# Kernel tuning notes

Measured on AMD Instinct MI355X. Metric: run time of the kernel, lower is better.

The kernel has to match this reference:

```python
import jax, jax.numpy as jnp
import numpy as np

X_DIM = 40
N_BATCH = 65536


def _circ_conv1d(x, W, b, pad):
    # x: [N, C_in, L], W: [C_out, C_in, K] (torch layout), circular padding
    if pad > 0:
        x = jnp.pad(x, ((0, 0), (0, 0), (pad, pad)), mode='wrap')
    y = jax.lax.conv_general_dilated(x, W, window_strides=(1,), padding='VALID',
                                     dimension_numbers=('NCH', 'OIH', 'NCH'))
    return y + b[None, :, None]


def setup_inputs() -> dict:
    key = jax.random.key(0)
    ks = jax.random.split(key, 9)
    u = jax.random.normal(ks[0], (N_BATCH, X_DIM), dtype=jnp.float32)
    coeff = jax.random.normal(ks[1], (18,), dtype=jnp.float32) * 0.1
    # Conv1d params, torch layout [out_ch, in_ch, kernel], kaiming-ish scale
    W1 = jax.random.normal(ks[2], (72, 1, 5), dtype=jnp.float32) * (1.0 / np.sqrt(1 * 5))
    b1 = jax.random.normal(ks[3], (72,), dtype=jnp.float32) * 0.05
    W2 = jax.random.normal(ks[4], (37, 48, 5), dtype=jnp.float32) * (1.0 / np.sqrt(48 * 5))
    b2 = jax.random.normal(ks[5], (37,), dtype=jnp.float32) * 0.05
    W3 = jax.random.normal(ks[6], (1, 37, 1), dtype=jnp.float32) * (1.0 / np.sqrt(37))
    b3 = jax.random.normal(ks[7], (1,), dtype=jnp.float32) * 0.05
    t = jnp.zeros((1,), dtype=jnp.float32)  # unused by the module, kept for signature fidelity
    return {"t": t, "u": u, "coeff": coeff, "W1": W1, "b1": b1,
            "W2": W2, "b2": b2, "W3": W3, "b3": b3}


def reference(t, u, coeff, W1, b1, W2, b2, W3, b3):
    # circular neighbor gathers: index_select with (i+k)%D == roll by -k
    u_m2 = jnp.roll(u, 2, axis=-1)
    u_m1 = jnp.roll(u, 1, axis=-1)
    u_p1 = jnp.roll(u, -1, axis=-1)
    u_p2 = jnp.roll(u, -2, axis=-1)
    feats = jnp.stack([
        jnp.ones_like(u),
        u_m2, u_m1, u, u_p1, u_p2,
        u_m2 ** 2, u_m1 ** 2, u ** 2, u_p1 ** 2, u_p2 ** 2,
        u_m2 * u_m1, u_m1 * u, u * u_p1, u_p1 * u_p2,
        u_m2 * u, u_m1 * u_p1, u * u_p2,
    ], axis=-1)  # [N, D, 18]
    out1 = feats @ coeff  # [N, D]

    x = u[:, None, :]  # [N, 1, D]
    h = jax.nn.relu(_circ_conv1d(x, W1, b1, 2))  # [N, 72, D]
    h = jnp.concatenate([h[:, :24], h[:, 24:48] * h[:, 48:]], axis=1)  # [N, 48, D]
    h = jax.nn.relu(_circ_conv1d(h, W2, b2, 2))  # [N, 37, D]
    out2 = _circ_conv1d(h, W3, b3, 0)[:, 0, :]  # [N, D]
    return out1 + out2
```

## Files before the change

### kernel.cpp

```cpp
#include <hip/hip_runtime.h>
#include <hip/hip_bf16.h>

typedef short s16x8 __attribute__((ext_vector_type(8)));
typedef short s16x4 __attribute__((ext_vector_type(4)));
typedef float f32x4 __attribute__((ext_vector_type(4)));

#define TB 8
#define NBG 4
#define HALO 46
#define GSTRIDE 2216
#define USTRIDE 50
#define NT 3
#define GT_SHORTS (TB * GSTRIDE)

__device__ __forceinline__ unsigned short f2bf(float f) {
    unsigned int u = __float_as_uint(f);
    u += 0x7fff + ((u >> 16) & 1);
    return (unsigned short)(u >> 16);
}

__device__ __forceinline__ unsigned int pk_bf16(float lo, float hi) {
    float2 f; f.x = lo; f.y = hi;
    __hip_bfloat162 h = __float22bfloat162_rn(f);
    union { __hip_bfloat162 b; unsigned int u; } c;
    c.b = h;
    return c.u;
}

__global__ __launch_bounds__(256, 2) void lorenz96_fused(
    const float* __restrict__ u,
    const float* __restrict__ coeff,
    const float* __restrict__ W1,
    const float* __restrict__ b1,
    const float* __restrict__ W2,
    const float* __restrict__ b2,
    const float* __restrict__ W3,
    const float* __restrict__ b3,
    float* __restrict__ out)
{
    __shared__ __align__(16) unsigned short gtile[GT_SHORTS];
    __shared__ __align__(16) float u_sbuf[2][TB * USTRIDE];
    __shared__ float out1_s[TB * 40];

    unsigned short* B_lds = gtile;

    const int t    = threadIdx.x;
    const int lane = t & 63;
    const int wave = t >> 6;
    const int quad = lane >> 4;
    const int l15  = lane & 15;

    const int b0_block = blockIdx.x * (TB * NBG);

    for (int g = t; g < NT * 8 * 64; g += 256) {
        int lg = g & 63;
        int ks = (g >> 6) & 7;
        int nt = g >> 9;
        int o  = nt * 16 + (lg & 15);
        int kb = ks * 32 + (lg >> 4) * 8;
        s16x8 pack = {0, 0, 0, 0, 0, 0, 0, 0};
        #pragma unroll
        for (int j = 0; j < 8; ++j) {
            int k = kb + j;
            if (k < 240 && o < 37) {
                int c = k % 48, tap = k / 48;
                pack[j] = (short)f2bf(W2[o * 240 + c * 5 + tap]);
            }
        }
        *(s16x8*)&B_lds[g * 8] = pack;
    }

    for (int idx = t; idx < TB * USTRIDE; idx += 256) {
        int b = idx / USTRIDE, k = idx - b * USTRIDE;
        int gi = k + 36; gi -= (gi >= 40) ? 40 : 0; gi -= (gi >= 40) ? 40 : 0;
        u_sbuf[0][idx] = u[(size_t)(b0_block + b) * 40 + gi];
    }

    s16x8 aW1[5];
    {
        int chs[5];
        chs[0] = l15; chs[1] = 16 + l15; chs[2] = 32 + l15;
        chs[3] = (l15 >= 8) ? 40 + l15 : -1;
        chs[4] = 56 + l15;
        #pragma unroll
        for (int mt = 0; mt < 5; ++mt) {
            s16x8 a = {0, 0, 0, 0, 0, 0, 0, 0};
            int ch = chs[mt];
            if (quad == 0 && ch >= 0) {
                #pragma unroll
                for (int j = 0; j < 5; ++j) a[j] = (short)f2bf(W1[ch * 5 + j]);
                a[5] = (short)f2bf(b1[ch]);
            }
            aW1[mt] = a;
        }
    }

    float w3v[NT][4], b2v[NT][4];
    #pragma unroll
    for (int nt = 0; nt < NT; ++nt)
        #pragma unroll
        for (int r = 0; r < 4; ++r) {
            int o = nt * 16 + quad * 4 + r;
            bool valid = (o < 37);
            w3v[nt][r] = valid ? W3[o] : 0.f;
            b2v[nt][r] = valid ? b2[o] : 0.f;
        }
    const float b3v = b3[0];
    float cf[18];
    #pragma unroll
    for (int i = 0; i < 18; ++i) cf[i] = coeff[i];

    __syncthreads();

    s16x8 aW2[NT][8];
    #pragma unroll
    for (int nt = 0; nt < NT; ++nt)
        #pragma unroll
        for (int ks = 0; ks < 8; ++ks)
            aW2[nt][ks] = *(const s16x8*)&B_lds[((nt * 8 + ks) * 64 + lane) * 8];

    for (int grp = 0; grp < NBG; ++grp) {
        const int b0 = b0_block + grp * TB;
        const float* u_s = u_sbuf[grp & 1];

        __syncthreads();

        {
            #pragma unroll
            for (int pass = 0; pass < 2; ++pass) {
                int i = pass ? 4 : quad;
                bool act = pass ? (quad == 0) : true;
                if (act) {
                    int m = (wave + 4 * i) * 16 + l15;
                    int p = m >> 3, b = m & 7;
                    const float* us = &u_s[b * USTRIDE + p];
                    float um2 = us[2], um1 = us[3], u0 = us[4], up1 = us[5], up2 = us[6];
                    float r = cf[0] + cf[1]*um2 + cf[2]*um1 + cf[3]*u0 + cf[4]*up1 + cf[5]*up2
                            + cf[6]*um2*um2 + cf[7]*um1*um1 + cf[8]*u0*u0 + cf[9]*up1*up1 + cf[10]*up2*up2
                            + cf[11]*um2*um1 + cf[12]*um1*u0 + cf[13]*u0*up1 + cf[14]*up1*up2
                            + cf[15]*um2*u0 + cf[16]*um1*up1 + cf[17]*u0*up2;
                    out1_s[m] = r;
                }
            }
        }

        #pragma unroll
        for (int i = 0; i < 6; ++i) {
            const int ct  = wave + 4 * i;
            const int col = ct * 16 + l15;
            const int b = col & 7, h = col >> 3;
            const int hc = (h < HALO) ? h : 0;
            s16x8 bU = {0, 0, 0, 0, 0, 0, 0, 0};
            if (quad == 0) {
                const float* us = &u_s[b * USTRIDE + hc];
                union { s16x8 v; unsigned int w[4]; } bu;
                bu.w[0] = pk_bf16(us[0], us[1]);
                bu.w[1] = pk_bf16(us[2], us[3]);
                bu.w[2] = pk_bf16(us[4], 1.0f);
                bu.w[3] = 0;
                bU = bu.v;
            }
            f32x4 a0 = {0.f,0.f,0.f,0.f}, a1 = a0, a2 = a0, a3 = a0, a4 = a0;
            a0 = __builtin_amdgcn_mfma_f32_16x16x32_bf16(aW1[0], bU, a0, 0, 0, 0);
            a1 = __builtin_amdgcn_mfma_f32_16x16x32_bf16(aW1[1], bU, a1, 0, 0, 0);
            a2 = __builtin_amdgcn_mfma_f32_16x16x32_bf16(aW1[2], bU, a2, 0, 0, 0);
            a3 = __builtin_amdgcn_mfma_f32_16x16x32_bf16(aW1[3], bU, a3, 0, 0, 0);
            a4 = __builtin_amdgcn_mfma_f32_16x16x32_bf16(aW1[4], bU, a4, 0, 0, 0);
            if (h < HALO) {
                float v0[4], v1[4], v2[4];
                #pragma unroll
                for (int r = 0; r < 4; ++r) {
                    v0[r] = fmaxf(a0[r], 0.f);
                    v1[r] = fmaxf(a1[r], 0.f);
                    if (quad >= 2) v1[r] *= fmaxf(a3[r], 0.f);
                    v2[r] = fmaxf(a2[r], 0.f) * fmaxf(a4[r], 0.f);
                }
                union { s16x4 v; unsigned int w[2]; } w0, w1, w2;
                w0.w[0] = pk_bf16(v0[0], v0[1]); w0.w[1] = pk_bf16(v0[2], v0[3]);
                w1.w[0] = pk_bf16(v1[0], v1[1]); w1.w[1] = pk_bf16(v1[2], v1[3]);
                w2.w[0] = pk_bf16(v2[0], v2[1]); w2.w[1] = pk_bf16(v2[2], v2[3]);
                unsigned short* gp = &gtile[b * GSTRIDE + h * 48 + quad * 4];
                *(s16x4*)(gp)      = w0.v;
                *(s16x4*)(gp + 16) = w1.v;
                *(s16x4*)(gp + 32) = w2.v;
            }
        }

        if (grp + 1 < NBG) {
            for (int idx = t; idx < TB * USTRIDE; idx += 256) {
                int b = idx / USTRIDE, k = idx - b * USTRIDE;
                int gi = k + 36; gi -= (gi >= 40) ? 40 : 0; gi -= (gi >= 40) ? 40 : 0;
                u_sbuf[(grp + 1) & 1][idx] = u[(size_t)(b0 + TB + b) * 40 + gi];
            }
        }

        __syncthreads();

        #pragma unroll
        for (int i = 0; i < 5; ++i) {
            const int mt = wave + 4 * i;
            const int m  = mt * 16 + l15;
            const int p  = m >> 3, b = m & 7;
            const unsigned short* gbase = &gtile[b * GSTRIDE + p * 48 + quad * 8];
            s16x8 bg[8];
            #pragma unroll
            for (int ks = 0; ks < 8; ++ks) bg[ks] = *(const s16x8*)(gbase + ks * 32);
            f32x4 c0 = {0.f,0.f,0.f,0.f}, c1 = c0, c2 = c0;
            #pragma unroll
            for (int ks = 0; ks < 8; ++ks) {
                c0 = __builtin_amdgcn_mfma_f32_16x16x32_bf16(aW2[0][ks], bg[ks], c0, 0, 0, 0);
                c1 = __builtin_amdgcn_mfma_f32_16x16x32_bf16(aW2[1][ks], bg[ks], c1, 0, 0, 0);
                c2 = __builtin_amdgcn_mfma_f32_16x16x32_bf16(aW2[2][ks], bg[ks], c2, 0, 0, 0);
            }
            float s = 0.f;
            #pragma unroll
            for (int r = 0; r < 4; ++r) {
                s += fmaxf(c0[r] + b2v[0][r], 0.f) * w3v[0][r];
                s += fmaxf(c1[r] + b2v[1][r], 0.f) * w3v[1][r];
                s += fmaxf(c2[r] + b2v[2][r], 0.f) * w3v[2][r];
            }
            s += __shfl_xor(s, 16, 64);
            s += __shfl_xor(s, 32, 64);
            if (lane < 16) {
                int mo = mt * 16 + lane;
                out[(size_t)(b0 + (mo & 7)) * 40 + (mo >> 3)] = s + b3v + out1_s[mo];
            }
        }
    }
}

extern "C" void kernel_launch(void* const* d_in, const int* in_sizes, int n_in,
                              void* d_out, int out_size, void* d_ws, size_t ws_size,
                              hipStream_t stream) {
    const float* u     = (const float*)d_in[1];
    const float* coeff = (const float*)d_in[2];
    const float* W1    = (const float*)d_in[3];
    const float* b1    = (const float*)d_in[4];
    const float* W2    = (const float*)d_in[5];
    const float* b2    = (const float*)d_in[6];
    const float* W3    = (const float*)d_in[7];
    const float* b3    = (const float*)d_in[8];
    float* out = (float*)d_out;

    const int n_batch = in_sizes[1] / 40;
    const int grid = n_batch / (TB * NBG);
    lorenz96_fused<<<grid, 256, 0, stream>>>(u, coeff, W1, b1, W2, b2, W3, b3, out);
}
```

Baseline: 211.1 us.

## Double-buffer conv intermediate tile and fold conv2 bias into MFMA

Double-buffers the LDS intermediate tile and the polynomial output, so the next group's conv1 stage is computed right after the current group's conv2 stage. This leaves one barrier per group instead of two. The conv2 bias is folded into the weight fragment at reduction index 240, with a bf16 1.0 injected into the B operand, which drops the per-element bias add. Each block now handles 8 batch groups instead of 4, amortizing weight setup over more work. The cost is double the LDS footprint, which may limit occupancy, and half as many blocks.

```diff
diff --git a/kernel.cpp b/kernel.cpp
--- a/kernel.cpp
+++ b/kernel.cpp
@@ -6,7 +6,7 @@
 typedef float f32x4 __attribute__((ext_vector_type(4)));
 
 #define TB 8
-#define NBG 4
+#define NBG 8
 #define HALO 46
 #define GSTRIDE 2216
 #define USTRIDE 50
@@ -38,11 +38,11 @@
     const float* __restrict__ b3,
     float* __restrict__ out)
 {
-    __shared__ __align__(16) unsigned short gtile[GT_SHORTS];
+    __shared__ __align__(16) unsigned short gtile[2][GT_SHORTS];
     __shared__ __align__(16) float u_sbuf[2][TB * USTRIDE];
-    __shared__ float out1_s[TB * 40];
-
-    unsigned short* B_lds = gtile;
+    __shared__ float out1_sb[2][TB * 40];
+
+    unsigned short* B_lds = &gtile[0][0];
 
     const int t    = threadIdx.x;
     const int lane = t & 63;
@@ -62,18 +62,16 @@
         #pragma unroll
         for (int j = 0; j < 8; ++j) {
             int k = kb + j;
-            if (k < 240 && o < 37) {
-                int c = k % 48, tap = k / 48;
-                pack[j] = (short)f2bf(W2[o * 240 + c * 5 + tap]);
+            if (o < 37) {
+                if (k < 240) {
+                    int c = k % 48, tap = k / 48;
+                    pack[j] = (short)f2bf(W2[o * 240 + c * 5 + tap]);
+                } else if (k == 240) {
+                    pack[j] = (short)f2bf(b2[o]);
+                }
             }
         }
         *(s16x8*)&B_lds[g * 8] = pack;
-    }
-
-    for (int idx = t; idx < TB * USTRIDE; idx += 256) {
-        int b = idx / USTRIDE, k = idx - b * USTRIDE;
-        int gi = k + 36; gi -= (gi >= 40) ? 40 : 0; gi -= (gi >= 40) ? 40 : 0;
-        u_sbuf[0][idx] = u[(size_t)(b0_block + b) * 40 + gi];
     }
 
     s16x8 aW1[5];
@@ -95,55 +93,51 @@
         }
     }
 
-    float w3v[NT][4], b2v[NT][4];
+    float w3v[NT][4];
     #pragma unroll
     for (int nt = 0; nt < NT; ++nt)
         #pragma unroll
         for (int r = 0; r < 4; ++r) {
             int o = nt * 16 + quad * 4 + r;
-            bool valid = (o < 37);
-            w3v[nt][r] = valid ? W3[o] : 0.f;
-            b2v[nt][r] = valid ? b2[o] : 0.f;
+            w3v[nt][r] = (o < 37) ? W3[o] : 0.f;
         }
     const float b3v = b3[0];
     float cf[18];
     #pragma unroll
     for (int i = 0; i < 18; ++i) cf[i] = coeff[i];
 
-    __syncthreads();
-
-    s16x8 aW2[NT][8];
-    #pragma unroll
-    for (int nt = 0; nt < NT; ++nt)
-        #pragma unroll
-        for (int ks = 0; ks < 8; ++ks)
-            aW2[nt][ks] = *(const s16x8*)&B_lds[((nt * 8 + ks) * 64 + lane) * 8];
-
-    for (int grp = 0; grp < NBG; ++grp) {
-        const int b0 = b0_block + grp * TB;
+    auto prestage_u = [&](int grp) {
+        for (int idx = t; idx < TB * USTRIDE; idx += 256) {
+            int b = idx / USTRIDE, k = idx - b * USTRIDE;
+            int gi = k + 36; gi -= (gi >= 40) ? 40 : 0; gi -= (gi >= 40) ? 40 : 0;
+            u_sbuf[grp & 1][idx] = u[(size_t)(b0_block + grp * TB + b) * 40 + gi];
+        }
+    };
+
+    auto poly = [&](int grp) {
         const float* u_s = u_sbuf[grp & 1];
-
-        __syncthreads();
-
-        {
-            #pragma unroll
-            for (int pass = 0; pass < 2; ++pass) {
-                int i = pass ? 4 : quad;
-                bool act = pass ? (quad == 0) : true;
-                if (act) {
-                    int m = (wave + 4 * i) * 16 + l15;
-                    int p = m >> 3, b = m & 7;
-                    const float* us = &u_s[b * USTRIDE + p];
-                    float um2 = us[2], um1 = us[3], u0 = us[4], up1 = us[5], up2 = us[6];
-                    float r = cf[0] + cf[1]*um2 + cf[2]*um1 + cf[3]*u0 + cf[4]*up1 + cf[5]*up2
-                            + cf[6]*um2*um2 + cf[7]*um1*um1 + cf[8]*u0*u0 + cf[9]*up1*up1 + cf[10]*up2*up2
-                            + cf[11]*um2*um1 + cf[12]*um1*u0 + cf[13]*u0*up1 + cf[14]*up1*up2
-                            + cf[15]*um2*u0 + cf[16]*um1*up1 + cf[17]*u0*up2;
-                    out1_s[m] = r;
-                }
-            }
-        }
-
+        float* o1 = out1_sb[grp & 1];
+        #pragma unroll
+        for (int pass = 0; pass < 2; ++pass) {
+            int i = pass ? 4 : quad;
+            bool act = pass ? (quad == 0) : true;
+            if (act) {
+                int m = (wave + 4 * i) * 16 + l15;
+                int p = m >> 3, b = m & 7;
+                const float* us = &u_s[b * USTRIDE + p];
+                float um2 = us[2], um1 = us[3], u0 = us[4], up1 = us[5], up2 = us[6];
+                float r = cf[0] + cf[1]*um2 + cf[2]*um1 + cf[3]*u0 + cf[4]*up1 + cf[5]*up2
+                        + cf[6]*um2*um2 + cf[7]*um1*um1 + cf[8]*u0*u0 + cf[9]*up1*up1 + cf[10]*up2*up2
+                        + cf[11]*um2*um1 + cf[12]*um1*u0 + cf[13]*u0*up1 + cf[14]*up1*up2
+                        + cf[15]*um2*u0 + cf[16]*um1*up1 + cf[17]*u0*up2;
+                o1[m] = r;
+            }
+        }
+    };
+
+    auto phase2 = [&](int grp) {
+        const float* u_s = u_sbuf[grp & 1];
+        unsigned short* gt = &gtile[grp & 1][0];
         #pragma unroll
         for (int i = 0; i < 6; ++i) {
             const int ct  = wave + 4 * i;
@@ -179,32 +173,50 @@
                 w0.w[0] = pk_bf16(v0[0], v0[1]); w0.w[1] = pk_bf16(v0[2], v0[3]);
                 w1.w[0] = pk_bf16(v1[0], v1[1]); w1.w[1] = pk_bf16(v1[2], v1[3]);
                 w2.w[0] = pk_bf16(v2[0], v2[1]); w2.w[1] = pk_bf16(v2[2], v2[3]);
-                unsigned short* gp = &gtile[b * GSTRIDE + h * 48 + quad * 4];
+                unsigned short* gp = &gt[b * GSTRIDE + h * 48 + quad * 4];
                 *(s16x4*)(gp)      = w0.v;
                 *(s16x4*)(gp + 16) = w1.v;
                 *(s16x4*)(gp + 32) = w2.v;
             }
         }
-
-        if (grp + 1 < NBG) {
-            for (int idx = t; idx < TB * USTRIDE; idx += 256) {
-                int b = idx / USTRIDE, k = idx - b * USTRIDE;
-                int gi = k + 36; gi -= (gi >= 40) ? 40 : 0; gi -= (gi >= 40) ? 40 : 0;
-                u_sbuf[(grp + 1) & 1][idx] = u[(size_t)(b0 + TB + b) * 40 + gi];
-            }
-        }
-
-        __syncthreads();
+    };
+
+    prestage_u(0);
+    __syncthreads();
+
+    s16x8 aW2[NT][8];
+    #pragma unroll
+    for (int nt = 0; nt < NT; ++nt)
+        #pragma unroll
+        for (int ks = 0; ks < 8; ++ks)
+            aW2[nt][ks] = *(const s16x8*)&B_lds[((nt * 8 + ks) * 64 + lane) * 8];
+
+    poly(0);
+    prestage_u(1);
+    __syncthreads();
+
+    phase2(0);
+    __syncthreads();
+
+    for (int g = 0; g < NBG; ++g) {
+        const int b0 = b0_block + g * TB;
+        const unsigned short* gt = &gtile[g & 1][0];
+        const float* o1 = out1_sb[g & 1];
 
         #pragma unroll
         for (int i = 0; i < 5; ++i) {
             const int mt = wave + 4 * i;
             const int m  = mt * 16 + l15;
             const int p  = m >> 3, b = m & 7;
-            const unsigned short* gbase = &gtile[b * GSTRIDE + p * 48 + quad * 8];
+            const unsigned short* gbase = &gt[b * GSTRIDE + p * 48 + quad * 8];
             s16x8 bg[8];
             #pragma unroll
             for (int ks = 0; ks < 8; ++ks) bg[ks] = *(const s16x8*)(gbase + ks * 32);
+            {
+                s16x8 b7 = bg[7];
+                if (quad == 2) b7[0] = (short)0x3F80;
+                bg[7] = b7;
+            }
             f32x4 c0 = {0.f,0.f,0.f,0.f}, c1 = c0, c2 = c0;
             #pragma unroll
             for (int ks = 0; ks < 8; ++ks) {
@@ -215,16 +227,23 @@
             float s = 0.f;
             #pragma unroll
             for (int r = 0; r < 4; ++r) {
-                s += fmaxf(c0[r] + b2v[0][r], 0.f) * w3v[0][r];
-                s += fmaxf(c1[r] + b2v[1][r], 0.f) * w3v[1][r];
-                s += fmaxf(c2[r] + b2v[2][r], 0.f) * w3v[2][r];
+                s += fmaxf(c0[r], 0.f) * w3v[0][r];
+                s += fmaxf(c1[r], 0.f) * w3v[1][r];
+                s += fmaxf(c2[r], 0.f) * w3v[2][r];
             }
             s += __shfl_xor(s, 16, 64);
             s += __shfl_xor(s, 32, 64);
             if (lane < 16) {
                 int mo = mt * 16 + lane;
-                out[(size_t)(b0 + (mo & 7)) * 40 + (mo >> 3)] = s + b3v + out1_s[mo];
-            }
+                out[(size_t)(b0 + (mo & 7)) * 40 + (mo >> 3)] = s + b3v + o1[mo];
+            }
+        }
+
+        if (g + 1 < NBG) {
+            poly(g + 1);
+            phase2(g + 1);
+            if (g + 2 < NBG) prestage_u(g + 2);
+            __syncthreads();
         }
     }
 }
```

After: 194.2 us. 8.0% less time.
